# Optimization experiments

Measured on AMD Instinct MI355X. Metric: run time of the kernel, lower is better.

The kernel has to match this reference:

```python
import jax, jax.numpy as jnp
import numpy as np

MODEL_DIM = 1024
NUM_HEADS = 16
K_DIM = MODEL_DIM // NUM_HEADS


def setup_inputs() -> dict:
    key = jax.random.key(0)
    kx, kw1, kw2 = jax.random.split(key, 3)
    B, L, D = 4, 2048, MODEL_DIM
    x = jax.random.normal(kx, (B, L, D), dtype=jnp.float32)
    # nn.Linear(D, 3D, bias=False): y = x @ W^T; store transposed form [D, 3D]
    scale1 = 1.0 / np.sqrt(D)
    Wqkv = jax.random.uniform(kw1, (D, 3 * D), dtype=jnp.float32, minval=-scale1, maxval=scale1)
    Wout = jax.random.uniform(kw2, (D, D), dtype=jnp.float32, minval=-scale1, maxval=scale1)
    return {"x": x, "Wqkv": Wqkv, "Wout": Wout}


def reference(x, Wqkv, Wout):
    B, L, D = x.shape
    H, Kd = NUM_HEADS, K_DIM
    qkv = x @ Wqkv  # [B, L, 3D]
    q, k, v = jnp.split(qkv, 3, axis=-1)

    def heads(t):  # [B, L, D] -> [B, H, L, Kd]
        return t.reshape(B, L, H, Kd).transpose(0, 2, 1, 3)

    qh, kh, vh = heads(q), heads(k), heads(v)
    scores = jnp.einsum('bhqd,bhkd->bhqk', qh, kh) / jnp.sqrt(jnp.float32(Kd))
    causal = jnp.triu(jnp.ones((L, L), dtype=bool), k=1)  # True above diagonal
    scores = jnp.where(causal, -jnp.inf, scores)
    probs = jax.nn.softmax(scores, axis=-1)
    attended = jnp.einsum('bhqk,bhkd->bhqd', probs, vh)
    concatted = attended.transpose(0, 2, 1, 3).reshape(B, L, D)
    # dropout is identity in eval mode
    return concatted @ Wout
```

## Files before the change

kernel.cpp:

```cpp
#include <hip/hip_runtime.h>

typedef unsigned short u16;
typedef unsigned int   u32;
typedef __bf16   bf16x8 __attribute__((ext_vector_type(8)));
typedef float    f32x4  __attribute__((ext_vector_type(4)));
typedef u16      u16x4  __attribute__((ext_vector_type(4)));
typedef u16      u16x8  __attribute__((ext_vector_type(8)));
typedef u32      u32x2  __attribute__((ext_vector_type(2)));
typedef u32      u32x4  __attribute__((ext_vector_type(4)));

#if __has_builtin(__builtin_amdgcn_exp2f)
#define EXP2(x) __builtin_amdgcn_exp2f(x)
#else
#define EXP2(x) exp2f(x)
#endif

__device__ __forceinline__ u16 f2bf(float f) {
    unsigned u = __float_as_uint(f);
    u += 0x7FFFu + ((u >> 16) & 1u);
    return (u16)(u >> 16);
}

__device__ __forceinline__ u32 pack_bf16(float a, float b) {
#if __has_builtin(__builtin_amdgcn_cvt_pk_bf16_f32)
    typedef __bf16 bf16x2 __attribute__((ext_vector_type(2)));
    bf16x2 r = __builtin_amdgcn_cvt_pk_bf16_f32(a, b);
    return __builtin_bit_cast(u32, r);
#else
    return (u32)f2bf(a) | ((u32)f2bf(b) << 16);
#endif
}

__device__ __forceinline__ void async_copy16(const u16* g, u16* l) {
    __builtin_amdgcn_global_load_lds(
        (const __attribute__((address_space(1))) unsigned*)g,
        (__attribute__((address_space(3))) unsigned*)l, 16, 0, 0);
}

__device__ __forceinline__ bf16x8 lds_frag(const u16* p) {
    return *(const bf16x8*)p;
}

__device__ __forceinline__ void permlane32_swap(u32& a, u32& b) {
    asm("v_permlane32_swap_b32 %0, %1" : "+v"(a), "+v"(b));
}
__device__ __forceinline__ void permlane16_swap(u32& a, u32& b) {
    asm("v_permlane16_swap_b32 %0, %1" : "+v"(a), "+v"(b));
}

__global__ __launch_bounds__(256) void prep(const float* __restrict__ x,
                                            const float* __restrict__ Wqkv,
                                            const float* __restrict__ Wout,
                                            u16* __restrict__ xb,
                                            u16* __restrict__ wqkv_t,
                                            u16* __restrict__ wout_t) {
    __shared__ u16 t[64 * 72];
    const int bid = blockIdx.x;
    const int tid = threadIdx.x;

    if (bid >= 1024) {
        size_t i = ((size_t)(bid - 1024) * 256 + tid) * 8;
        float4 v0 = *(const float4*)(x + i);
        float4 v1 = *(const float4*)(x + i + 4);
        u16x8 o = { f2bf(v0.x), f2bf(v0.y), f2bf(v0.z), f2bf(v0.w),
                    f2bf(v1.x), f2bf(v1.y), f2bf(v1.z), f2bf(v1.w) };
        *(u16x8*)(xb + i) = o;
        return;
    }

    const float* W;  u16* Wt;  int Kd, Nd, n0, k0;
    if (bid < 768) { W = Wqkv; Wt = wqkv_t; Kd = 1024; Nd = 3072;
                     n0 = (bid % 48) * 64; k0 = (bid / 48) * 64; }
    else           { W = Wout; Wt = wout_t; Kd = 1024; Nd = 1024;
                     n0 = ((bid - 768) % 16) * 64; k0 = ((bid - 768) / 16) * 64; }
#pragma unroll
    for (int i = 0; i < 4; ++i) {
        int lin = i * 256 + tid;
        int kr = lin >> 4, nc = (lin & 15) << 2;
        float4 v = *(const float4*)(W + (size_t)(k0 + kr) * Nd + n0 + nc);
        u16x4 o = { f2bf(v.x), f2bf(v.y), f2bf(v.z), f2bf(v.w) };
        *(u16x4*)&t[kr * 72 + nc] = o;
    }
    __syncthreads();
#pragma unroll
    for (int i = 0; i < 2; ++i) {
        int lin = i * 256 + tid;
        int nr = lin >> 3, kc = (lin & 7) << 3;
        u16x8 o;
#pragma unroll
        for (int jj = 0; jj < 8; ++jj) o[jj] = t[(kc + jj) * 72 + nr];
        *(u16x8*)(Wt + (size_t)(n0 + nr) * Kd + k0 + kc) = o;
    }
}

__global__ __launch_bounds__(256) void gemm_qkv(const u16* __restrict__ A,
                                                const u16* __restrict__ Bt,
                                                u16* __restrict__ outb,
                                                int K, int N) {
    __shared__ u16 As[2][128 * 32];
    __shared__ u16 Bs[2][128 * 32];
    const int tid = threadIdx.x;
    const int lane = tid & 63;
    const int wv = tid >> 6;
    const int wr = (wv >> 1) * 64;
    const int wc = (wv & 1) * 64;
    const int qd = lane >> 4;
    const int c  = lane & 15;

    const int flat = blockIdx.x;
    const int r_ = flat & 7;
    const int q_ = flat >> 3;
    const int m0 = ((r_ >> 1) * 16 + q_ / 12) * 128;
    const int n0 = ((r_ & 1) * 12 + q_ % 12) * 128;

    const int srow = tid >> 2;
    const int sg = ((tid & 3) ^ ((srow >> 1) & 3)) << 3;

    const u16* Ag0 = A  + (size_t)(m0 +      srow) * K + sg;
    const u16* Ag1 = A  + (size_t)(m0 + 64 + srow) * K + sg;
    const u16* Bg0 = Bt + (size_t)(n0 +      srow) * K + sg;
    const u16* Bg1 = Bt + (size_t)(n0 + 64 + srow) * K + sg;

    const u32 fsw = (qd ^ ((c >> 1) & 3)) << 3;
    const u32 a_off = (wr + c) * 32 + fsw;
    const u32 b_off = (wc + c) * 32 + fsw;

    f32x4 acc[4][4] = {};

    async_copy16(Ag0, &As[0][tid * 8]);
    async_copy16(Ag1, &As[0][2048 + tid * 8]);
    async_copy16(Bg0, &Bs[0][tid * 8]);
    async_copy16(Bg1, &Bs[0][2048 + tid * 8]);

    int p = 0;
    for (int k0 = 0; k0 < K; k0 += 32) {
        __syncthreads();
        if (k0 + 32 < K) {
            const int np = p ^ 1;
            async_copy16(Ag0 + k0 + 32, &As[np][tid * 8]);
            async_copy16(Ag1 + k0 + 32, &As[np][2048 + tid * 8]);
            async_copy16(Bg0 + k0 + 32, &Bs[np][tid * 8]);
            async_copy16(Bg1 + k0 + 32, &Bs[np][2048 + tid * 8]);
        }
        bf16x8 af[4], bfr[4];
#pragma unroll
        for (int i = 0; i < 4; ++i) af[i]  = lds_frag(&As[p][a_off + i * 512]);
#pragma unroll
        for (int j = 0; j < 4; ++j) bfr[j] = lds_frag(&Bs[p][b_off + j * 512]);
#pragma unroll
        for (int i = 0; i < 4; ++i)
#pragma unroll
            for (int j = 0; j < 4; ++j)
                acc[i][j] = __builtin_amdgcn_mfma_f32_16x16x32_bf16(af[i], bfr[j], acc[i][j], 0, 0, 0);
        p ^= 1;
    }

#pragma unroll
    for (int i = 0; i < 4; ++i)
#pragma unroll
        for (int j = 0; j < 4; ++j) {
            int n = n0 + wc + j * 16 + c;
            int which = n >> 10, h = (n >> 6) & 15, kd = n & 63;
            int m_base = m0 + wr + i * 16 + qd * 4;
            int b = m_base >> 11, l0 = m_base & 2047;
            int bh = b * 16 + h;
            if (which == 2) {
                u32x2 o2;
                o2[0] = pack_bf16(acc[i][j][0], acc[i][j][1]);
                o2[1] = pack_bf16(acc[i][j][2], acc[i][j][3]);
                *(u32x2*)(outb + (size_t)(128 + bh) * 131072 + (size_t)kd * 2048 + l0) = o2;
            } else if (which == 0) {
#pragma unroll
                for (int r = 0; r < 4; ++r)
                    outb[(size_t)bh * 131072 + (size_t)(l0 + r) * 64 + kd] =
                        f2bf(acc[i][j][r] * 0.1803368801f);
            } else {
#pragma unroll
                for (int r = 0; r < 4; ++r)
                    outb[(size_t)(64 + bh) * 131072 + (size_t)(l0 + r) * 64 + kd] =
                        f2bf(acc[i][j][r]);
            }
        }
}

__global__ __launch_bounds__(256) void gemm_out(const u16* __restrict__ A,
                                                const u16* __restrict__ Bt,
                                                float* __restrict__ outf,
                                                int K, int N) {
    __shared__ u16 As[2][128 * 64];
    __shared__ u16 Bs[2][128 * 64];
    const int tid = threadIdx.x;
    const int lane = tid & 63;
    const int wv = tid >> 6;
    const int wr = (wv >> 1) * 64;
    const int wc = (wv & 1) * 64;
    const int qd = lane >> 4;
    const int c  = lane & 15;

    const int flat = blockIdx.x;
    const int r_ = flat & 7;
    const int q_ = flat >> 3;
    const int m0 = (r_ * 8 + (q_ >> 3)) * 128;
    const int n0 = (q_ & 7) * 128;

    auto stage = [&](int t, int slot) {
        const int kb = t * 64;
#pragma unroll
        for (int it = 0; it < 4; ++it) {
            int lin = it * 256 + tid;
            int row = lin >> 3;
            int sch = ((lin & 7) ^ (row & 7)) << 3;
            async_copy16(A  + (size_t)(m0 + row) * K + kb + sch,
                         &As[slot][lin * 8]);
            async_copy16(Bt + (size_t)(n0 + row) * K + kb + sch,
                         &Bs[slot][lin * 8]);
        }
    };

    const u32 a_base = (wr + c) * 64;
    const u32 b_base = (wc + c) * 64;
    const u32 ch0 = (u32)((qd ^ (c & 7)) << 3);
    const u32 ch1 = (u32)(((4 + qd) ^ (c & 7)) << 3);

    f32x4 acc[4][4] = {};

    stage(0, 0);

    const int NT = K >> 6;
    int p = 0;
#pragma unroll 1
    for (int kt = 0; kt < NT; ++kt) {
        __syncthreads();
        if (kt + 1 < NT) stage(kt + 1, p ^ 1);

        bf16x8 af[4], bfr[4];
#pragma unroll
        for (int i = 0; i < 4; ++i) af[i]  = lds_frag(&As[p][a_base + i * 1024 + ch0]);
#pragma unroll
        for (int j = 0; j < 4; ++j) bfr[j] = lds_frag(&Bs[p][b_base + j * 1024 + ch0]);
#pragma unroll
        for (int i = 0; i < 4; ++i)
#pragma unroll
            for (int j = 0; j < 4; ++j)
                acc[i][j] = __builtin_amdgcn_mfma_f32_16x16x32_bf16(af[i], bfr[j], acc[i][j], 0, 0, 0);
#pragma unroll
        for (int i = 0; i < 4; ++i) af[i]  = lds_frag(&As[p][a_base + i * 1024 + ch1]);
#pragma unroll
        for (int j = 0; j < 4; ++j) bfr[j] = lds_frag(&Bs[p][b_base + j * 1024 + ch1]);
#pragma unroll
        for (int i = 0; i < 4; ++i)
#pragma unroll
            for (int j = 0; j < 4; ++j)
                acc[i][j] = __builtin_amdgcn_mfma_f32_16x16x32_bf16(af[i], bfr[j], acc[i][j], 0, 0, 0);
        p ^= 1;
    }

#pragma unroll
    for (int i = 0; i < 4; ++i)
#pragma unroll
        for (int j = 0; j < 4; ++j) {
            int n = n0 + wc + j * 16 + c;
            int m_base = m0 + wr + i * 16 + qd * 4;
#pragma unroll
            for (int r = 0; r < 4; ++r)
                outf[(size_t)(m_base + r) * N + n] = acc[i][j][r];
        }
}

#define ATTN_S(KSB, QA, QB)                                                   \
    do {                                                                      \
        _Pragma("unroll") for (int f = 0; f < 8; ++f) {                       \
            sa[f] = f32x4{-8.f, -8.f, -8.f, -8.f};                            \
            sb[f] = f32x4{-8.f, -8.f, -8.f, -8.f};                            \
        }                                                                     \
        __builtin_amdgcn_s_setprio(1);                                        \
        _Pragma("unroll") for (int ks = 0; ks < 2; ++ks) {                    \
            const u16* kp = (KSB) + kf_off[ks];                               \
            _Pragma("unroll") for (int f = 0; f < 8; ++f) {                   \
                bf16x8 kf = lds_frag(kp + f * 1024);                          \
                sa[f] = __builtin_amdgcn_mfma_f32_16x16x32_bf16(              \
                    kf, QA[ks], sa[f], 0, 0, 0);                              \
                sb[f] = __builtin_amdgcn_mfma_f32_16x16x32_bf16(              \
                    kf, QB[ks], sb[f], 0, 0, 0);                              \
            }                                                                 \
        }                                                                     \
        __builtin_amdgcn_s_setprio(0);                                        \
    } while (0)

#define ATTN_FIN(VTB, KT, QT, QAROW, QBROW, RVA, RVB, ACCA, ACCB)             \
    do {                                                                      \
        if ((KT) == (QT)) {                                                   \
            _Pragma("unroll") for (int f = 0; f < 8; ++f)                     \
                _Pragma("unroll") for (int r = 0; r < 4; ++r) {               \
                    int key = (KT) * 128 + f * 16 + qd * 4 + r;               \
                    if (key > (QAROW)) sa[f][r] = -3e38f;                     \
                    if (key > (QBROW)) sb[f][r] = -3e38f;                     \
                }                                                             \
        }                                                                     \
        _Pragma("unroll") for (int f = 0; f < 8; ++f) {                       \
            _Pragma("unroll") for (int r = 0; r < 4; ++r) {                   \
                sa[f][r] = EXP2(sa[f][r]);                                    \
                sb[f][r] = EXP2(sb[f][r]);                                    \
            }                                                                 \
            RVA += sa[f];                                                     \
            RVB += sb[f];                                                     \
        }                                                                     \
        _Pragma("unroll") for (int kc = 0; kc < 4; ++kc) {                    \
            u32 a0 = pack_bf16(sa[2 * kc][0], sa[2 * kc][1]);                 \
            u32 a1 = pack_bf16(sa[2 * kc + 1][0], sa[2 * kc + 1][1]);         \
            u32 b0 = pack_bf16(sa[2 * kc][2], sa[2 * kc][3]);                 \
            u32 b1 = pack_bf16(sa[2 * kc + 1][2], sa[2 * kc + 1][3]);         \
            permlane32_swap(a0, a1); permlane16_swap(a0, a1);                 \
            permlane32_swap(b0, b1); permlane16_swap(b0, b1);                 \
            u32x4 wpa = {a0, b0, a1, b1};                                     \
            bf16x8 pa = __builtin_bit_cast(bf16x8, wpa);                      \
            u32 c0 = pack_bf16(sb[2 * kc][0], sb[2 * kc][1]);                 \
            u32 c1 = pack_bf16(sb[2 * kc + 1][0], sb[2 * kc + 1][1]);         \
            u32 d0 = pack_bf16(sb[2 * kc][2], sb[2 * kc][3]);                 \
            u32 d1 = pack_bf16(sb[2 * kc + 1][2], sb[2 * kc + 1][3]);         \
            permlane32_swap(c0, c1); permlane16_swap(c0, c1);                 \
            permlane32_swap(d0, d1); permlane16_swap(d0, d1);                 \
            u32x4 wpb = {c0, d0, c1, d1};                                     \
            bf16x8 pb = __builtin_bit_cast(bf16x8, wpb);                      \
            const u16* vp = (VTB) + vf_off[kc];                               \
            __builtin_amdgcn_s_setprio(1);                                    \
            _Pragma("unroll") for (int jo = 0; jo < 4; ++jo) {                \
                bf16x8 vf = lds_frag(vp + jo * 2048);                         \
                ACCA[jo] = __builtin_amdgcn_mfma_f32_16x16x32_bf16(           \
                    vf, pa, ACCA[jo], 0, 0, 0);                               \
                ACCB[jo] = __builtin_amdgcn_mfma_f32_16x16x32_bf16(           \
                    vf, pb, ACCB[jo], 0, 0, 0);                               \
            }                                                                 \
            __builtin_amdgcn_s_setprio(0);                                    \
        }                                                                     \
    } while (0)

__global__ __launch_bounds__(256, 2) void attn_kernel(const u16* __restrict__ qkv,
                                                      u16* __restrict__ att) {
    __shared__ u16 Ks[2][128 * 64];
    __shared__ u16 Vt[2][64 * 128];

    const int tid = threadIdx.x;
    const int lane = tid & 63;
    const int w = tid >> 6;
    const int qd = lane >> 4;
    const int c = lane & 15;

    const int flat = blockIdx.x + 8 * blockIdx.y;
    const int bh = (flat & 7) + 8 * ((flat >> 3) & 7);
    const int bx = flat >> 6;
    const int b = bh >> 4, h = bh & 15;

    const u16* Qg = qkv + (size_t)bh * 131072;
    const u16* Kg = qkv + (size_t)(64 + bh) * 131072;
    const u16* Vg = qkv + (size_t)(128 + bh) * 131072;

    u32 kf_off[2];
#pragma unroll
    for (int ks = 0; ks < 2; ++ks)
        kf_off[ks] = c * 64 + (((ks * 4 + qd) ^ (c & 7)) << 3);
    u32 vf_off[4];
#pragma unroll
    for (int kc = 0; kc < 4; ++kc)
        vf_off[kc] = c * 128 + (((kc * 4 + qd) ^ c) << 3);

    auto issue_copy = [&](int t, u16* kd, u16* vd) {
#pragma unroll
        for (int it = 0; it < 4; ++it) {
            int lin = it * 256 + tid;
            int krw = lin >> 3, kch = lin & 7;
            int vrw = lin >> 4, vch = lin & 15;
            async_copy16(Kg + (size_t)t * 8192 + krw * 64 + ((kch ^ (krw & 7)) << 3),
                         kd + lin * 8);
            async_copy16(Vg + (size_t)t * 128 + (size_t)vrw * 2048 + ((vch ^ (vrw & 15)) << 3),
                         vd + lin * 8);
        }
    };

    const int qt0 = bx;
    const int qt1 = 15 - bx;
    const int NT  = qt1 + 1;

    const int qa0_row = qt0 * 128 + w * 32 + c;
    const int qb0_row = qa0_row + 16;
    const int qa1_row = qt1 * 128 + w * 32 + c;
    const int qb1_row = qa1_row + 16;

    bf16x8 qa0[2], qb0[2], qa1[2], qb1[2];
#pragma unroll
    for (int ks = 0; ks < 2; ++ks) {
        qa0[ks] = *(const bf16x8*)(Qg + (size_t)qa0_row * 64 + ks * 32 + qd * 8);
        qb0[ks] = *(const bf16x8*)(Qg + (size_t)qb0_row * 64 + ks * 32 + qd * 8);
        qa1[ks] = *(const bf16x8*)(Qg + (size_t)qa1_row * 64 + ks * 32 + qd * 8);
        qb1[ks] = *(const bf16x8*)(Qg + (size_t)qb1_row * 64 + ks * 32 + qd * 8);
    }

    f32x4 aa0[4] = {}, ab0[4] = {}, aa1[4] = {}, ab1[4] = {};
    f32x4 rva0 = {}, rvb0 = {}, rva1 = {}, rvb1 = {};
    f32x4 sa[8], sb[8];

    issue_copy(0, Ks[0], Vt[0]);
    __syncthreads();
    if (NT > 1) issue_copy(1, Ks[1], Vt[1]);

#pragma unroll 1
    for (int kt = 0; kt < NT; ++kt) {
        const int p = kt & 1;
        if (kt <= qt0) {
            ATTN_S(Ks[p], qa0, qb0);
            ATTN_FIN(Vt[p], kt, qt0, qa0_row, qb0_row, rva0, rvb0, aa0, ab0);
        }
        ATTN_S(Ks[p], qa1, qb1);
        ATTN_FIN(Vt[p], kt, qt1, qa1_row, qb1_row, rva1, rvb1, aa1, ab1);
        if (kt + 1 < NT) {
            __syncthreads();
            if (kt + 2 < NT) issue_copy(kt + 2, Ks[p], Vt[p]);
        }
    }

#pragma unroll
    for (int sgi = 0; sgi < 2; ++sgi) {
        f32x4* Aa = sgi ? aa1 : aa0;
        f32x4* Ab = sgi ? ab1 : ab0;
        f32x4 rv_a = sgi ? rva1 : rva0;
        f32x4 rv_b = sgi ? rvb1 : rvb0;
        int ra_row = sgi ? qa1_row : qa0_row;
        int rb_row = sgi ? qb1_row : qb0_row;
        float ra = rv_a[0] + rv_a[1] + rv_a[2] + rv_a[3];
        float rb = rv_b[0] + rv_b[1] + rv_b[2] + rv_b[3];
        ra += __shfl_xor(ra, 16, 64);
        ra += __shfl_xor(ra, 32, 64);
        rb += __shfl_xor(rb, 16, 64);
        rb += __shfl_xor(rb, 32, 64);
        float ia = __builtin_amdgcn_rcpf(ra), ib = __builtin_amdgcn_rcpf(rb);
        u16* ar = att + ((size_t)b * 2048 + ra_row) * 1024 + h * 64;
        u16* br = att + ((size_t)b * 2048 + rb_row) * 1024 + h * 64;
#pragma unroll
        for (int jo = 0; jo < 4; ++jo) {
            u32x2 oa, ob;
            oa[0] = pack_bf16(Aa[jo][0] * ia, Aa[jo][1] * ia);
            oa[1] = pack_bf16(Aa[jo][2] * ia, Aa[jo][3] * ia);
            ob[0] = pack_bf16(Ab[jo][0] * ib, Ab[jo][1] * ib);
            ob[1] = pack_bf16(Ab[jo][2] * ib, Ab[jo][3] * ib);
            *(u32x2*)(ar + jo * 16 + qd * 4) = oa;
            *(u32x2*)(br + jo * 16 + qd * 4) = ob;
        }
    }
}

extern "C" void kernel_launch(void* const* d_in, const int* in_sizes, int n_in,
                              void* d_out, int out_size, void* d_ws, size_t ws_size,
                              hipStream_t stream) {
    const float* x    = (const float*)d_in[0];
    const float* Wqkv = (const float*)d_in[1];
    const float* Wout = (const float*)d_in[2];
    float* out = (float*)d_out;

    char* ws = (char*)d_ws;
    u16* x_bf   = (u16*)(ws);
    u16* wqkv_t = (u16*)(ws + 16777216);
    u16* wout_t = (u16*)(ws + 23068672);
    u16* qkv_h  = (u16*)(ws + 25165824);
    u16* att    = (u16*)(ws + 75497472);

    prep<<<dim3(5120), dim3(256), 0, stream>>>(x, Wqkv, Wout, x_bf, wqkv_t, wout_t);
    gemm_qkv<<<dim3(1536), dim3(256), 0, stream>>>(x_bf, wqkv_t, qkv_h, 1024, 3072);
    attn_kernel<<<dim3(8, 64), dim3(256), 0, stream>>>(qkv_h, att);
    gemm_out<<<dim3(512), dim3(256), 0, stream>>>(att, wout_t, out, 1024, 1024);
}
```

Baseline: 236.3 us.

## Split attention into one query tile per block and drop double-buffered K/V

Each attention block now handles a single 128-row query tile instead of a paired light/heavy tile pair, which doubles the grid to 1024 blocks. Blocks are ordered by an interleaved index so tile sizes are spread across the grid. Shared memory drops to a single K/V buffer and the launch_bounds occupancy hint is removed. The aim is more parallelism and lower per-block LDS and register pressure, but the synchronous copy-then-compute loop gives up the previous overlap of loads with compute, and K/V tiles are now fetched twice as often.

```diff
diff --git a/kernel.cpp b/kernel.cpp
--- a/kernel.cpp
+++ b/kernel.cpp
@@ -335,10 +335,10 @@
         }                                                                     \
     } while (0)
 
-__global__ __launch_bounds__(256, 2) void attn_kernel(const u16* __restrict__ qkv,
-                                                      u16* __restrict__ att) {
-    __shared__ u16 Ks[2][128 * 64];
-    __shared__ u16 Vt[2][64 * 128];
+__global__ __launch_bounds__(256) void attn_kernel(const u16* __restrict__ qkv,
+                                                   u16* __restrict__ att) {
+    __shared__ u16 Ks[128 * 64];
+    __shared__ u16 Vt[64 * 128];
 
     const int tid = threadIdx.x;
     const int lane = tid & 63;
@@ -346,9 +346,11 @@
     const int qd = lane >> 4;
     const int c = lane & 15;
 
-    const int flat = blockIdx.x + 8 * blockIdx.y;
-    const int bh = (flat & 7) + 8 * ((flat >> 3) & 7);
-    const int bx = flat >> 6;
+    const int idx = blockIdx.x;
+    const int g = idx >> 8;
+    const int s = (idx >> 6) & 3;
+    const int bh = idx & 63;
+    const int qt = (g & 1) ? (15 - 2 * s - (g >> 1)) : (2 * s + (g >> 1));
     const int b = bh >> 4, h = bh & 15;
 
     const u16* Qg = qkv + (size_t)bh * 131072;
@@ -364,87 +366,62 @@
     for (int kc = 0; kc < 4; ++kc)
         vf_off[kc] = c * 128 + (((kc * 4 + qd) ^ c) << 3);
 
-    auto issue_copy = [&](int t, u16* kd, u16* vd) {
+    auto issue_copy = [&](int t) {
 #pragma unroll
         for (int it = 0; it < 4; ++it) {
             int lin = it * 256 + tid;
             int krw = lin >> 3, kch = lin & 7;
             int vrw = lin >> 4, vch = lin & 15;
             async_copy16(Kg + (size_t)t * 8192 + krw * 64 + ((kch ^ (krw & 7)) << 3),
-                         kd + lin * 8);
+                         Ks + lin * 8);
             async_copy16(Vg + (size_t)t * 128 + (size_t)vrw * 2048 + ((vch ^ (vrw & 15)) << 3),
-                         vd + lin * 8);
+                         Vt + lin * 8);
         }
     };
 
-    const int qt0 = bx;
-    const int qt1 = 15 - bx;
-    const int NT  = qt1 + 1;
-
-    const int qa0_row = qt0 * 128 + w * 32 + c;
-    const int qb0_row = qa0_row + 16;
-    const int qa1_row = qt1 * 128 + w * 32 + c;
-    const int qb1_row = qa1_row + 16;
-
-    bf16x8 qa0[2], qb0[2], qa1[2], qb1[2];
+    const int NT = qt + 1;
+
+    const int qa_row = qt * 128 + w * 32 + c;
+    const int qb_row = qa_row + 16;
+
+    bf16x8 qa[2], qb[2];
 #pragma unroll
     for (int ks = 0; ks < 2; ++ks) {
-        qa0[ks] = *(const bf16x8*)(Qg + (size_t)qa0_row * 64 + ks * 32 + qd * 8);
-        qb0[ks] = *(const bf16x8*)(Qg + (size_t)qb0_row * 64 + ks * 32 + qd * 8);
-        qa1[ks] = *(const bf16x8*)(Qg + (size_t)qa1_row * 64 + ks * 32 + qd * 8);
-        qb1[ks] = *(const bf16x8*)(Qg + (size_t)qb1_row * 64 + ks * 32 + qd * 8);
-    }
-
-    f32x4 aa0[4] = {}, ab0[4] = {}, aa1[4] = {}, ab1[4] = {};
-    f32x4 rva0 = {}, rvb0 = {}, rva1 = {}, rvb1 = {};
+        qa[ks] = *(const bf16x8*)(Qg + (size_t)qa_row * 64 + ks * 32 + qd * 8);
+        qb[ks] = *(const bf16x8*)(Qg + (size_t)qb_row * 64 + ks * 32 + qd * 8);
+    }
+
+    f32x4 acca[4] = {}, accb[4] = {};
+    f32x4 rva = {}, rvb = {};
     f32x4 sa[8], sb[8];
-
-    issue_copy(0, Ks[0], Vt[0]);
-    __syncthreads();
-    if (NT > 1) issue_copy(1, Ks[1], Vt[1]);
 
 #pragma unroll 1
     for (int kt = 0; kt < NT; ++kt) {
-        const int p = kt & 1;
-        if (kt <= qt0) {
-            ATTN_S(Ks[p], qa0, qb0);
-            ATTN_FIN(Vt[p], kt, qt0, qa0_row, qb0_row, rva0, rvb0, aa0, ab0);
-        }
-        ATTN_S(Ks[p], qa1, qb1);
-        ATTN_FIN(Vt[p], kt, qt1, qa1_row, qb1_row, rva1, rvb1, aa1, ab1);
-        if (kt + 1 < NT) {
-            __syncthreads();
-            if (kt + 2 < NT) issue_copy(kt + 2, Ks[p], Vt[p]);
-        }
-    }
-
-#pragma unroll
-    for (int sgi = 0; sgi < 2; ++sgi) {
-        f32x4* Aa = sgi ? aa1 : aa0;
-        f32x4* Ab = sgi ? ab1 : ab0;
-        f32x4 rv_a = sgi ? rva1 : rva0;
-        f32x4 rv_b = sgi ? rvb1 : rvb0;
-        int ra_row = sgi ? qa1_row : qa0_row;
-        int rb_row = sgi ? qb1_row : qb0_row;
-        float ra = rv_a[0] + rv_a[1] + rv_a[2] + rv_a[3];
-        float rb = rv_b[0] + rv_b[1] + rv_b[2] + rv_b[3];
-        ra += __shfl_xor(ra, 16, 64);
-        ra += __shfl_xor(ra, 32, 64);
-        rb += __shfl_xor(rb, 16, 64);
-        rb += __shfl_xor(rb, 32, 64);
-        float ia = __builtin_amdgcn_rcpf(ra), ib = __builtin_amdgcn_rcpf(rb);
-        u16* ar = att + ((size_t)b * 2048 + ra_row) * 1024 + h * 64;
-        u16* br = att + ((size_t)b * 2048 + rb_row) * 1024 + h * 64;
-#pragma unroll
-        for (int jo = 0; jo < 4; ++jo) {
-            u32x2 oa, ob;
-            oa[0] = pack_bf16(Aa[jo][0] * ia, Aa[jo][1] * ia);
-            oa[1] = pack_bf16(Aa[jo][2] * ia, Aa[jo][3] * ia);
-            ob[0] = pack_bf16(Ab[jo][0] * ib, Ab[jo][1] * ib);
-            ob[1] = pack_bf16(Ab[jo][2] * ib, Ab[jo][3] * ib);
-            *(u32x2*)(ar + jo * 16 + qd * 4) = oa;
-            *(u32x2*)(br + jo * 16 + qd * 4) = ob;
-        }
+        issue_copy(kt);
+        __syncthreads();
+        ATTN_S(Ks, qa, qb);
+        ATTN_FIN(Vt, kt, qt, qa_row, qb_row, rva, rvb, acca, accb);
+        if (kt + 1 < NT) __syncthreads();
+    }
+
+    float ra = rva[0] + rva[1] + rva[2] + rva[3];
+    float rb = rvb[0] + rvb[1] + rvb[2] + rvb[3];
+    ra += __shfl_xor(ra, 16, 64);
+    ra += __shfl_xor(ra, 32, 64);
+    rb += __shfl_xor(rb, 16, 64);
+    rb += __shfl_xor(rb, 32, 64);
+    float ia = __builtin_amdgcn_rcpf(ra), ib = __builtin_amdgcn_rcpf(rb);
+    u16* ar = att + ((size_t)b * 2048 + qa_row) * 1024 + h * 64;
+    u16* br = att + ((size_t)b * 2048 + qb_row) * 1024 + h * 64;
+#pragma unroll
+    for (int jo = 0; jo < 4; ++jo) {
+        u32x2 oa, ob;
+        oa[0] = pack_bf16(acca[jo][0] * ia, acca[jo][1] * ia);
+        oa[1] = pack_bf16(acca[jo][2] * ia, acca[jo][3] * ia);
+        ob[0] = pack_bf16(accb[jo][0] * ib, accb[jo][1] * ib);
+        ob[1] = pack_bf16(accb[jo][2] * ib, accb[jo][3] * ib);
+        *(u32x2*)(ar + jo * 16 + qd * 4) = oa;
+        *(u32x2*)(br + jo * 16 + qd * 4) = ob;
     }
 }
 
@@ -465,6 +442,6 @@
 
     prep<<<dim3(5120), dim3(256), 0, stream>>>(x, Wqkv, Wout, x_bf, wqkv_t, wout_t);
     gemm_qkv<<<dim3(1536), dim3(256), 0, stream>>>(x_bf, wqkv_t, qkv_h, 1024, 3072);
-    attn_kernel<<<dim3(8, 64), dim3(256), 0, stream>>>(qkv_h, att);
+    attn_kernel<<<dim3(1024), dim3(256), 0, stream>>>(qkv_h, att);
     gemm_out<<<dim3(512), dim3(256), 0, stream>>>(att, wout_t, out, 1024, 1024);
 }
```

Result: slower. 249.3 us (+5.5%).
